# Kernel tuning notes

Measured on AMD Instinct MI355X. Metric: run time of the kernel, lower is better.

Reference implementation:

```python
import jax, jax.numpy as jnp
import numpy as np

B, S_SRC, S_TGT = 32, 128, 128
V, E, H = 32000, 256, 256
PAD_ID = 0
NEG = -1.0e9


def setup_inputs() -> dict:
    key = jax.random.key(0)
    ks = jax.random.split(key, 16)
    lengths_de = jax.random.randint(ks[0], (B,), S_SRC // 2, S_SRC + 1)
    idx_de = jax.random.randint(ks[1], (B, S_SRC), 1, V)
    pos = jnp.arange(S_SRC)[None, :]
    indices_de = jnp.where(pos < lengths_de[:, None], idx_de, PAD_ID)
    indices_en = jax.random.randint(ks[2], (B, S_TGT), 1, V)
    lengths_en = jnp.full((B,), S_TGT, dtype=jnp.int32)

    sc = 0.02
    def nrm(k, shape):
        return jax.random.normal(k, shape, dtype=jnp.float32) * sc
    emb_enc = nrm(ks[3], (V, E)).at[PAD_ID].set(0.0)
    emb_dec = nrm(ks[4], (V, E)).at[PAD_ID].set(0.0)
    return {
        "indices_de": indices_de, "lengths_de": lengths_de,
        "indices_en": indices_en, "lengths_en": lengths_en,
        "emb_enc": emb_enc, "emb_dec": emb_dec,
        "W_ih_enc": nrm(ks[5], (H, E)), "W_hh_enc": nrm(ks[6], (H, H)),
        "b_ih_enc": jnp.zeros((H,), jnp.float32), "b_hh_enc": jnp.zeros((H,), jnp.float32),
        "W_ih_dec": nrm(ks[7], (H, E)), "W_hh_dec": nrm(ks[8], (H, H)),
        "b_ih_dec": jnp.zeros((H,), jnp.float32), "b_hh_dec": jnp.zeros((H,), jnp.float32),
        "W_attn": nrm(ks[9], (H, 2 * H)), "b_attn": jnp.zeros((H,), jnp.float32),
        "W_out": nrm(ks[10], (V, H)), "b_out": jnp.zeros((V,), jnp.float32),
    }


def reference(indices_de, lengths_de, indices_en, lengths_en,
              emb_enc, emb_dec,
              W_ih_enc, W_hh_enc, b_ih_enc, b_hh_enc,
              W_ih_dec, W_hh_dec, b_ih_dec, b_hh_dec,
              W_attn, b_attn, W_out, b_out):
    # ---- Encoder: tanh RNN over packed sequence ----
    x_enc = emb_enc[indices_de]                      # [B, S, E]
    valid = jnp.arange(S_SRC)[None, :] < lengths_de[:, None]  # [B, S]

    def enc_step(h, inp):
        x_t, v_t = inp                                # [B,E], [B]
        h_new = jnp.tanh(x_t @ W_ih_enc.T + b_ih_enc + h @ W_hh_enc.T + b_hh_enc)
        h = jnp.where(v_t[:, None], h_new, h)         # frozen past length (pack semantics)
        out = jnp.where(v_t[:, None], h_new, 0.0)     # padded outputs are zero
        return h, out

    h0 = jnp.zeros((B, H), jnp.float32)
    h_final, enc_outs = jax.lax.scan(
        enc_step, h0, (x_enc.transpose(1, 0, 2), valid.T))
    encoder_outputs = enc_outs.transpose(1, 0, 2)     # [B, S, H]
    enc_mask = indices_de == PAD_ID                   # [B, S] True at padding

    # ---- Decoder: per-step RNN cell + dot-product attention + vocab proj ----
    x_dec = emb_dec[indices_en]                       # [B, T, E]

    def dec_step(h, x_t):
        h = jnp.tanh(x_t @ W_ih_dec.T + b_ih_dec + h @ W_hh_dec.T + b_hh_dec)
        scores = jnp.einsum('bh,bsh->bs', h, encoder_outputs)
        scores = jnp.where(enc_mask, NEG, scores)
        attn = jax.nn.softmax(scores, axis=-1)
        context = jnp.einsum('bs,bsh->bh', attn, encoder_outputs)
        combined = jnp.concatenate([context, h], axis=1)          # [B, 2H]
        attn_out = jnp.tanh(combined @ W_attn.T + b_attn)         # [B, H]
        logits_t = attn_out @ W_out.T + b_out                     # [B, V]
        return h, logits_t

    _, logits = jax.lax.scan(dec_step, h_final, x_dec.transpose(1, 0, 2))
    return logits.transpose(1, 0, 2)                  # [B, T, V]
```

## Files before the change

kernel.cpp:

```cpp
#include <hip/hip_runtime.h>
#include <stdint.h>

#define B_ 32
#define S_ 128
#define T_ 128
#define V_ 32000
#define E_ 256
#define H_ 256
#define NEG_ (-1.0e9f)

typedef __attribute__((ext_vector_type(8))) short short8;
typedef __attribute__((ext_vector_type(4))) float floatx4;

__device__ __forceinline__ unsigned short f2bf(float x){
  unsigned u = __float_as_uint(x);
  u = u + 0x7fffu + ((u >> 16) & 1u);
  return (unsigned short)(u >> 16);
}
__device__ __forceinline__ float bf2f(unsigned short s){
  return __uint_as_float(((unsigned)s) << 16);
}
__device__ __forceinline__ float hsum4(float4 v){ return (v.x+v.y)+(v.z+v.w); }
__device__ __forceinline__ void unpack8(uint4 q, float4& lo, float4& hi){
  lo.x = __uint_as_float(q.x << 16); lo.y = __uint_as_float(q.x & 0xffff0000u);
  lo.z = __uint_as_float(q.y << 16); lo.w = __uint_as_float(q.y & 0xffff0000u);
  hi.x = __uint_as_float(q.z << 16); hi.y = __uint_as_float(q.z & 0xffff0000u);
  hi.z = __uint_as_float(q.w << 16); hi.w = __uint_as_float(q.w & 0xffff0000u);
}

#define GLOAD_LDS16(gptr, lptr) \
  __builtin_amdgcn_global_load_lds( \
      (const __attribute__((address_space(1))) unsigned int*)(const void*)(gptr), \
      (__attribute__((address_space(3))) unsigned int*)(void*)(lptr), 16, 0, 0)

__global__ void k_cvt(const float* __restrict__ src, unsigned short* __restrict__ dst, int n4){
  int i = blockIdx.x*256 + threadIdx.x;
  if (i < n4){
    float4 v = ((const float4*)src)[i];
    ushort4 o; o.x=f2bf(v.x); o.y=f2bf(v.y); o.z=f2bf(v.z); o.w=f2bf(v.w);
    ((ushort4*)dst)[i] = o;
  }
}

__global__ __launch_bounds__(256) void k_xih(
    const int* __restrict__ idxmat,
    const float* __restrict__ emb,
    const float* __restrict__ Wih,
    const float* __restrict__ b1, const float* __restrict__ b2,
    float* __restrict__ out)
{
  __shared__ int idx_s[16];
  __shared__ float4 x_s[16][64];
  int b = blockIdx.x >> 3;
  int t0 = (blockIdx.x & 7) << 4;
  int tid = threadIdx.x;
  if (tid < 16) idx_s[tid] = idxmat[b*128 + t0 + tid];
  __syncthreads();
  for (int r = 0; r < 16; ++r)
    ((float*)&x_s[r][0])[tid] = emb[(size_t)idx_s[r]*E_ + tid];
  __syncthreads();
  int j2 = tid & 127, tg = tid >> 7;
  const float4* W0 = (const float4*)(Wih + (size_t)j2*E_);
  const float4* W1 = (const float4*)(Wih + (size_t)(j2+128)*E_);
  float4 a0[8], a1[8];
  #pragma unroll
  for (int t=0;t<8;++t){ a0[t]={0,0,0,0}; a1[t]={0,0,0,0}; }
  for (int e4 = 0; e4 < 64; ++e4){
    float4 w0 = W0[e4], w1 = W1[e4];
    #pragma unroll
    for (int t = 0; t < 8; ++t){
      float4 xv = x_s[tg*8+t][e4];
      a0[t] += w0*xv; a1[t] += w1*xv;
    }
  }
  float bi0 = b1[j2] + b2[j2];
  float bi1 = b1[j2+128] + b2[j2+128];
  #pragma unroll
  for (int t = 0; t < 8; ++t){
    size_t row = (size_t)((b<<7) + t0 + tg*8 + t)*H_;
    out[row + j2]     = hsum4(a0[t]) + bi0;
    out[row + j2+128] = hsum4(a1[t]) + bi1;
  }
}

template<int ENC>
__global__ __launch_bounds__(512, 2) void k_rnn(
    const float* __restrict__ Whh,
    const float* __restrict__ Xih,
    const float* __restrict__ h0,
    const int* __restrict__ lengths,
    unsigned short* __restrict__ enc_out,
    float* __restrict__ hseq,
    float* __restrict__ hfinal)
{
  __shared__ float4 h4_s[64];
  __shared__ float part[2][256];
  float* h_s = (float*)h4_s;
  int b = blockIdx.x, tid = threadIdx.x;
  int j = tid & 255, half = tid >> 8;
  float4 w[32];
  const float4* Wr = (const float4*)(Whh + (size_t)j*H_ + half*128);
  #pragma unroll
  for (int i = 0; i < 32; ++i) w[i] = Wr[i];
  if (tid < 256) h_s[tid] = ENC ? 0.f : h0[b*H_ + tid];
  int len = ENC ? lengths[b] : T_;
  __syncthreads();
  for (int t = 0; t < 128; ++t){
    float x = 0.f;
    if (tid < 256) x = Xih[(size_t)((b<<7) + t)*H_ + j];
    const float4* hh = h4_s + (half << 5);
    float4 acc0 = {0,0,0,0}, acc1 = {0,0,0,0};
    #pragma unroll
    for (int i = 0; i < 32; i += 2){ acc0 += w[i]*hh[i]; acc1 += w[i+1]*hh[i+1]; }
    part[half][j] = hsum4(acc0) + hsum4(acc1);
    __syncthreads();
    if (tid < 256){
      float s = x + part[0][tid] + part[1][tid];
      float hn = tanhf(s);
      if (ENC){
        float hold = h_s[tid];
        bool v = (t < len);
        h_s[tid] = v ? hn : hold;
        enc_out[(size_t)((b<<7)+t)*H_ + tid] = f2bf(v ? hn : 0.f);
      } else {
        h_s[tid] = hn;
        hseq[(size_t)((b<<7)+t)*H_ + tid] = hn;
      }
    }
    __syncthreads();
  }
  if (ENC && tid < 256) hfinal[b*H_ + tid] = h_s[tid];
}

__global__ __launch_bounds__(256) void k_attn(
    const unsigned short* __restrict__ enc_out,
    const float* __restrict__ hseq,
    const int* __restrict__ lengths,
    const unsigned short* __restrict__ Wattn,
    const float* __restrict__ battn,
    unsigned short* __restrict__ attn_out)
{
  __shared__ float h_sm[16][256];
  __shared__ float sc[16][132];
  __shared__ float comb[16][512];
  int bx = blockIdx.x; int b = bx >> 3; int t0 = (bx & 7) << 4;
  int tid = threadIdx.x;
  int len = lengths[b];
  for (int r = 0; r < 16; ++r)
    h_sm[r][tid] = hseq[(size_t)((b<<7) + t0 + r)*H_ + tid];
  __syncthreads();
  {
    int s = tid & 127, tg = tid >> 7;
    float4 a[8];
    #pragma unroll
    for (int t=0;t<8;++t) a[t] = {0,0,0,0};
    const uint4* ep = (const uint4*)(enc_out + (size_t)(b*S_ + s)*H_);
    for (int oct = 0; oct < 32; ++oct){
      uint4 q = ep[oct];
      float4 elo, ehi; unpack8(q, elo, ehi);
      #pragma unroll
      for (int t = 0; t < 8; ++t){
        const float4* hp = (const float4*)&h_sm[tg*8+t][oct*8];
        a[t] += elo*hp[0] + ehi*hp[1];
      }
    }
    #pragma unroll
    for (int t = 0; t < 8; ++t)
      sc[tg*8+t][s] = (s < len) ? hsum4(a[t]) : NEG_;
  }
  __syncthreads();
  {
    int wv = tid >> 6, ln = tid & 63;
    for (int r = 0; r < 4; ++r){
      int t = r*4 + wv;
      float v0 = sc[t][ln], v1 = sc[t][ln+64];
      float m = fmaxf(v0, v1);
      #pragma unroll
      for (int off = 32; off >= 1; off >>= 1) m = fmaxf(m, __shfl_xor(m, off));
      float e0 = __expf(v0 - m), e1 = __expf(v1 - m);
      float su = e0 + e1;
      #pragma unroll
      for (int off = 32; off >= 1; off >>= 1) su += __shfl_xor(su, off);
      float inv = 1.0f / su;
      sc[t][ln] = e0*inv; sc[t][ln+64] = e1*inv;
    }
  }
  __syncthreads();
  {
    int hd = tid & 127, tg = tid >> 7;
    float c0[8], c1[8];
    #pragma unroll
    for (int t=0;t<8;++t){ c0[t]=0.f; c1[t]=0.f; }
    for (int s4 = 0; s4 < 32; ++s4){
      float ea[4], eb[4];
      #pragma unroll
      for (int i = 0; i < 4; ++i){
        const unsigned short* er = enc_out + (size_t)(b*S_ + s4*4 + i)*H_;
        ea[i] = bf2f(er[hd]); eb[i] = bf2f(er[hd+128]);
      }
      #pragma unroll
      for (int t = 0; t < 8; ++t){
        float4 av = *(const float4*)&sc[tg*8+t][s4*4];
        c0[t] += av.x*ea[0] + av.y*ea[1] + av.z*ea[2] + av.w*ea[3];
        c1[t] += av.x*eb[0] + av.y*eb[1] + av.z*eb[2] + av.w*eb[3];
      }
    }
    #pragma unroll
    for (int t = 0; t < 8; ++t){
      comb[tg*8+t][hd]     = c0[t];
      comb[tg*8+t][hd+128] = c1[t];
    }
  }
  for (int r = 0; r < 16; ++r) comb[r][256 + tid] = h_sm[r][tid];
  __syncthreads();
  {
    int j2 = tid & 127, tg = tid >> 7;
    float4 a0[8], a1[8];
    #pragma unroll
    for (int t=0;t<8;++t){ a0[t]={0,0,0,0}; a1[t]={0,0,0,0}; }
    const uint4* W0 = (const uint4*)(Wattn + (size_t)j2*512);
    const uint4* W1 = (const uint4*)(Wattn + (size_t)(j2+128)*512);
    for (int oct = 0; oct < 64; ++oct){
      float4 w0lo, w0hi, w1lo, w1hi;
      unpack8(W0[oct], w0lo, w0hi);
      unpack8(W1[oct], w1lo, w1hi);
      #pragma unroll
      for (int t = 0; t < 8; ++t){
        const float4* cp = (const float4*)&comb[tg*8+t][oct*8];
        float4 clo = cp[0], chi = cp[1];
        a0[t] += w0lo*clo + w0hi*chi;
        a1[t] += w1lo*clo + w1hi*chi;
      }
    }
    float bi0 = battn[j2], bi1 = battn[j2+128];
    #pragma unroll
    for (int t = 0; t < 8; ++t){
      size_t row = (size_t)((b<<7) + t0 + tg*8 + t)*H_;
      attn_out[row + j2]     = f2bf(tanhf(hsum4(a0[t]) + bi0));
      attn_out[row + j2+128] = f2bf(tanhf(hsum4(a1[t]) + bi1));
    }
  }
}

__global__ __launch_bounds__(256) void k_vocab(
    const unsigned short* __restrict__ A,
    const unsigned short* __restrict__ Wb,
    const float* __restrict__ bout,
    float* __restrict__ out)
{
  __shared__ unsigned short Asm[2][128*32];
  __shared__ unsigned short Bsm[2][128*32];
  int nb = blockIdx.x, mb = blockIdx.y;
  int tid = threadIdx.x;
  int ln  = tid & 63;
  int wid = tid >> 6;
  int llo = ln & 15, lhi = ln >> 4;
  int wr = wid >> 1, wc = wid & 1;
  int mbase = mb*128, nbase = nb*128;

  int c0 = tid, c1 = tid + 256;
  int r0 = c0 >> 2, s0 = (c0 & 3) ^ ((r0 >> 1) & 3);
  int r1 = c1 >> 2, s1 = (c1 & 3) ^ ((r1 >> 1) & 3);
  const unsigned short* Ag0 = A  + (size_t)(mbase + r0)*256 + s0*8;
  const unsigned short* Ag1 = A  + (size_t)(mbase + r1)*256 + s1*8;
  const unsigned short* Bg0 = Wb + (size_t)(nbase + r0)*256 + s0*8;
  const unsigned short* Bg1 = Wb + (size_t)(nbase + r1)*256 + s1*8;

#define STAGE_V(bufi, kk) do { \
    GLOAD_LDS16(Ag0 + (kk), &Asm[bufi][c0*8]); \
    GLOAD_LDS16(Ag1 + (kk), &Asm[bufi][c1*8]); \
    GLOAD_LDS16(Bg0 + (kk), &Bsm[bufi][c0*8]); \
    GLOAD_LDS16(Bg1 + (kk), &Bsm[bufi][c1*8]); \
  } while(0)

  floatx4 acc[4][4];
  #pragma unroll
  for (int mi=0;mi<4;++mi)
    #pragma unroll
    for (int ni=0;ni<4;++ni) acc[mi][ni] = (floatx4){0.f,0.f,0.f,0.f};

  int q = (llo >> 1) & 3;
  int aoff[4], boff[4];
  #pragma unroll
  for (int i=0;i<4;++i){
    int arow = wr*64 + i*16 + llo;
    aoff[i] = arow*32 + ((lhi ^ q)*8);
    int brow = wc*64 + i*16 + llo;
    boff[i] = brow*32 + ((lhi ^ q)*8);
  }

  STAGE_V(0, 0);
  __syncthreads();

  #pragma unroll
  for (int k0 = 0; k0 < 8; ++k0){
    int cur = k0 & 1;
    if (k0 < 7) STAGE_V(cur^1, (k0+1)*32);
    short8 afr[4];
    #pragma unroll
    for (int mi=0;mi<4;++mi)
      afr[mi] = *(const short8*)&Asm[cur][aoff[mi]];
    #pragma unroll
    for (int ni=0;ni<4;++ni){
      short8 bfr = *(const short8*)&Bsm[cur][boff[ni]];
      #pragma unroll
      for (int mi=0;mi<4;++mi)
        acc[mi][ni] = __builtin_amdgcn_mfma_f32_16x16x32_bf16(afr[mi], bfr, acc[mi][ni], 0, 0, 0);
    }
    __syncthreads();
  }

  #pragma unroll
  for (int ni = 0; ni < 4; ++ni){
    int col = nbase + wc*64 + ni*16 + llo;
    float bias = bout[col];
    #pragma unroll
    for (int mi = 0; mi < 4; ++mi){
      #pragma unroll
      for (int r = 0; r < 4; ++r){
        int row = mbase + wr*64 + mi*16 + lhi*4 + r;
        out[(size_t)row*V_ + col] = acc[mi][ni][r] + bias;
      }
    }
  }
#undef STAGE_V
}

extern "C" void kernel_launch(void* const* d_in, const int* in_sizes, int n_in,
                              void* d_out, int out_size, void* d_ws, size_t ws_size,
                              hipStream_t stream){
  const int*   indices_de = (const int*)d_in[0];
  const int*   lengths_de = (const int*)d_in[1];
  const int*   indices_en = (const int*)d_in[2];
  const float* emb_enc   = (const float*)d_in[4];
  const float* emb_dec   = (const float*)d_in[5];
  const float* W_ih_enc  = (const float*)d_in[6];
  const float* W_hh_enc  = (const float*)d_in[7];
  const float* b_ih_enc  = (const float*)d_in[8];
  const float* b_hh_enc  = (const float*)d_in[9];
  const float* W_ih_dec  = (const float*)d_in[10];
  const float* W_hh_dec  = (const float*)d_in[11];
  const float* b_ih_dec  = (const float*)d_in[12];
  const float* b_hh_dec  = (const float*)d_in[13];
  const float* W_attn    = (const float*)d_in[14];
  const float* b_attn    = (const float*)d_in[15];
  const float* W_out     = (const float*)d_in[16];
  const float* b_out     = (const float*)d_in[17];

  char* ws = (char*)d_ws;
  size_t o = 0;
  float* Xih_enc = (float*)(ws + o); o += (size_t)4096*256*4;
  float* Xih_dec = (float*)(ws + o); o += (size_t)4096*256*4;
  unsigned short* enc_bf = (unsigned short*)(ws + o); o += (size_t)4096*256*2;
  float* hfinal  = (float*)(ws + o); o += (size_t)32*256*4;
  float* hdec    = (float*)(ws + o); o += (size_t)4096*256*4;
  unsigned short* attn_o  = (unsigned short*)(ws + o); o += (size_t)4096*256*2;
  unsigned short* Wout_bf = (unsigned short*)(ws + o); o += (size_t)V_*256*2;
  unsigned short* Wattn_bf= (unsigned short*)(ws + o); o += (size_t)256*512*2;

  k_cvt<<<8000, 256, 0, stream>>>(W_out, Wout_bf, 2048000);
  k_cvt<<<128, 256, 0, stream>>>(W_attn, Wattn_bf, 32768);
  k_xih<<<256, 256, 0, stream>>>(indices_de, emb_enc, W_ih_enc, b_ih_enc, b_hh_enc, Xih_enc);
  k_xih<<<256, 256, 0, stream>>>(indices_en, emb_dec, W_ih_dec, b_ih_dec, b_hh_dec, Xih_dec);
  k_rnn<1><<<32, 512, 0, stream>>>(W_hh_enc, Xih_enc, nullptr, lengths_de, enc_bf, nullptr, hfinal);
  k_rnn<0><<<32, 512, 0, stream>>>(W_hh_dec, Xih_dec, hfinal, nullptr, nullptr, hdec, nullptr);
  k_attn<<<256, 256, 0, stream>>>(enc_bf, hdec, lengths_de, Wattn_bf, b_attn, attn_o);
  dim3 gD(250, 32);
  k_vocab<<<gD, 256, 0, stream>>>(attn_o, Wout_bf, b_out, (float*)d_out);
}
```

Baseline: 995.0 us.

## Merge prep and RNN launches, enlarge vocab GEMM tile with XCD-aware mapping

Folds the two weight conversions and the two input-projection kernels into one launch, with the block index choosing the work. Runs the encoder and decoder recurrences in a single kernel, so the hidden state passes through shared memory instead of a global hfinal buffer. The per-step barriers become a manual waitcnt plus s_barrier. The vocab GEMM moves to 512-thread blocks with 256x128 tiles on a 1D grid, grouping M-blocks by XCD so each XCD can reuse W_out in L2. The larger tile and block size may reduce occupancy.

```diff
diff --git a/kernel.cpp b/kernel.cpp
--- a/kernel.cpp
+++ b/kernel.cpp
@@ -33,8 +33,15 @@
       (const __attribute__((address_space(1))) unsigned int*)(const void*)(gptr), \
       (__attribute__((address_space(3))) unsigned int*)(void*)(lptr), 16, 0, 0)
 
-__global__ void k_cvt(const float* __restrict__ src, unsigned short* __restrict__ dst, int n4){
-  int i = blockIdx.x*256 + threadIdx.x;
+#define LDS_BARRIER() do { \
+    asm volatile("s_waitcnt lgkmcnt(0)" ::: "memory"); \
+    __builtin_amdgcn_s_barrier(); \
+  } while(0)
+
+__device__ __forceinline__ void cvt_body(const float* __restrict__ src,
+                                         unsigned short* __restrict__ dst,
+                                         int blk, int n4){
+  int i = blk*256 + (int)threadIdx.x;
   if (i < n4){
     float4 v = ((const float4*)src)[i];
     ushort4 o; o.x=f2bf(v.x); o.y=f2bf(v.y); o.z=f2bf(v.z); o.w=f2bf(v.w);
@@ -42,17 +49,15 @@
   }
 }
 
-__global__ __launch_bounds__(256) void k_xih(
-    const int* __restrict__ idxmat,
-    const float* __restrict__ emb,
+__device__ __forceinline__ void xih_body(
+    const int* __restrict__ idxmat, const float* __restrict__ emb,
     const float* __restrict__ Wih,
     const float* __restrict__ b1, const float* __restrict__ b2,
-    float* __restrict__ out)
+    float* __restrict__ out, int blk,
+    int* idx_s, float4 (*x_s)[64])
 {
-  __shared__ int idx_s[16];
-  __shared__ float4 x_s[16][64];
-  int b = blockIdx.x >> 3;
-  int t0 = (blockIdx.x & 7) << 4;
+  int b = blk >> 3;
+  int t0 = (blk & 7) << 4;
   int tid = threadIdx.x;
   if (tid < 16) idx_s[tid] = idxmat[b*128 + t0 + tid];
   __syncthreads();
@@ -83,15 +88,38 @@
   }
 }
 
-template<int ENC>
-__global__ __launch_bounds__(512, 2) void k_rnn(
-    const float* __restrict__ Whh,
-    const float* __restrict__ Xih,
-    const float* __restrict__ h0,
+__global__ __launch_bounds__(256) void k_prep(
+    const float* __restrict__ W_out, unsigned short* __restrict__ Wout_bf,
+    const float* __restrict__ W_attn, unsigned short* __restrict__ Wattn_bf,
+    const int* __restrict__ indices_de, const float* __restrict__ emb_enc,
+    const float* __restrict__ W_ih_enc, const float* __restrict__ b_ih_enc,
+    const float* __restrict__ b_hh_enc, float* __restrict__ Xih_enc,
+    const int* __restrict__ indices_en, const float* __restrict__ emb_dec,
+    const float* __restrict__ W_ih_dec, const float* __restrict__ b_ih_dec,
+    const float* __restrict__ b_hh_dec, float* __restrict__ Xih_dec)
+{
+  __shared__ int idx_s[16];
+  __shared__ float4 x_s[16][64];
+  int bx = blockIdx.x;
+  if (bx < 8000){
+    cvt_body(W_out, Wout_bf, bx, 2048000);
+  } else if (bx < 8128){
+    cvt_body(W_attn, Wattn_bf, bx - 8000, 32768);
+  } else if (bx < 8384){
+    xih_body(indices_de, emb_enc, W_ih_enc, b_ih_enc, b_hh_enc, Xih_enc,
+             bx - 8128, idx_s, x_s);
+  } else {
+    xih_body(indices_en, emb_dec, W_ih_dec, b_ih_dec, b_hh_dec, Xih_dec,
+             bx - 8384, idx_s, x_s);
+  }
+}
+
+__global__ __launch_bounds__(512, 2) void k_rnn2(
+    const float* __restrict__ Whh_e, const float* __restrict__ Whh_d,
+    const float* __restrict__ Xih_e, const float* __restrict__ Xih_d,
     const int* __restrict__ lengths,
     unsigned short* __restrict__ enc_out,
-    float* __restrict__ hseq,
-    float* __restrict__ hfinal)
+    float* __restrict__ hseq)
 {
   __shared__ float4 h4_s[64];
   __shared__ float part[2][256];
@@ -99,37 +127,53 @@
   int b = blockIdx.x, tid = threadIdx.x;
   int j = tid & 255, half = tid >> 8;
   float4 w[32];
-  const float4* Wr = (const float4*)(Whh + (size_t)j*H_ + half*128);
+  const float4* Wr = (const float4*)(Whh_e + (size_t)j*H_ + half*128);
   #pragma unroll
   for (int i = 0; i < 32; ++i) w[i] = Wr[i];
-  if (tid < 256) h_s[tid] = ENC ? 0.f : h0[b*H_ + tid];
-  int len = ENC ? lengths[b] : T_;
-  __syncthreads();
+  if (tid < 256) h_s[tid] = 0.f;
+  int len = lengths[b];
+  __syncthreads();
+
   for (int t = 0; t < 128; ++t){
     float x = 0.f;
-    if (tid < 256) x = Xih[(size_t)((b<<7) + t)*H_ + j];
+    if (tid < 256) x = Xih_e[(size_t)((b<<7) + t)*H_ + j];
     const float4* hh = h4_s + (half << 5);
     float4 acc0 = {0,0,0,0}, acc1 = {0,0,0,0};
     #pragma unroll
     for (int i = 0; i < 32; i += 2){ acc0 += w[i]*hh[i]; acc1 += w[i+1]*hh[i+1]; }
     part[half][j] = hsum4(acc0) + hsum4(acc1);
-    __syncthreads();
+    LDS_BARRIER();
     if (tid < 256){
       float s = x + part[0][tid] + part[1][tid];
       float hn = tanhf(s);
-      if (ENC){
-        float hold = h_s[tid];
-        bool v = (t < len);
-        h_s[tid] = v ? hn : hold;
-        enc_out[(size_t)((b<<7)+t)*H_ + tid] = f2bf(v ? hn : 0.f);
-      } else {
-        h_s[tid] = hn;
-        hseq[(size_t)((b<<7)+t)*H_ + tid] = hn;
-      }
-    }
-    __syncthreads();
-  }
-  if (ENC && tid < 256) hfinal[b*H_ + tid] = h_s[tid];
+      float hold = h_s[tid];
+      bool v = (t < len);
+      h_s[tid] = v ? hn : hold;
+      enc_out[(size_t)((b<<7)+t)*H_ + tid] = f2bf(v ? hn : 0.f);
+    }
+    LDS_BARRIER();
+  }
+
+  Wr = (const float4*)(Whh_d + (size_t)j*H_ + half*128);
+  #pragma unroll
+  for (int i = 0; i < 32; ++i) w[i] = Wr[i];
+  for (int t = 0; t < 128; ++t){
+    float x = 0.f;
+    if (tid < 256) x = Xih_d[(size_t)((b<<7) + t)*H_ + j];
+    const float4* hh = h4_s + (half << 5);
+    float4 acc0 = {0,0,0,0}, acc1 = {0,0,0,0};
+    #pragma unroll
+    for (int i = 0; i < 32; i += 2){ acc0 += w[i]*hh[i]; acc1 += w[i+1]*hh[i+1]; }
+    part[half][j] = hsum4(acc0) + hsum4(acc1);
+    LDS_BARRIER();
+    if (tid < 256){
+      float s = x + part[0][tid] + part[1][tid];
+      float hn = tanhf(s);
+      h_s[tid] = hn;
+      hseq[(size_t)((b<<7)+t)*H_ + tid] = hn;
+    }
+    LDS_BARRIER();
+  }
 }
 
 __global__ __launch_bounds__(256) void k_attn(
@@ -242,35 +286,37 @@
   }
 }
 
-__global__ __launch_bounds__(256) void k_vocab(
+__global__ __launch_bounds__(512) void k_vocab(
     const unsigned short* __restrict__ A,
     const unsigned short* __restrict__ Wb,
     const float* __restrict__ bout,
     float* __restrict__ out)
 {
-  __shared__ unsigned short Asm[2][128*32];
-  __shared__ unsigned short Bsm[2][128*32];
-  int nb = blockIdx.x, mb = blockIdx.y;
+  __shared__ alignas(16) unsigned short Asm[2][256*32];
+  __shared__ alignas(16) unsigned short Bsm[2][128*32];
+  int bid = blockIdx.x;
+  int xcd = bid & 7, idx = bid >> 3;
+  int nb = idx >> 1;
+  int mb = (xcd << 1) | (idx & 1);
   int tid = threadIdx.x;
   int ln  = tid & 63;
   int wid = tid >> 6;
   int llo = ln & 15, lhi = ln >> 4;
   int wr = wid >> 1, wc = wid & 1;
-  int mbase = mb*128, nbase = nb*128;
-
-  int c0 = tid, c1 = tid + 256;
-  int r0 = c0 >> 2, s0 = (c0 & 3) ^ ((r0 >> 1) & 3);
-  int r1 = c1 >> 2, s1 = (c1 & 3) ^ ((r1 >> 1) & 3);
-  const unsigned short* Ag0 = A  + (size_t)(mbase + r0)*256 + s0*8;
-  const unsigned short* Ag1 = A  + (size_t)(mbase + r1)*256 + s1*8;
-  const unsigned short* Bg0 = Wb + (size_t)(nbase + r0)*256 + s0*8;
-  const unsigned short* Bg1 = Wb + (size_t)(nbase + r1)*256 + s1*8;
+  int mbase = mb*256, nbase = nb*128;
+
+  int ca0 = tid, ca1 = tid + 512, cb = tid;
+  int ra0 = ca0 >> 2, sa0 = (ca0 & 3) ^ ((ra0 >> 1) & 3);
+  int ra1 = ca1 >> 2, sa1 = (ca1 & 3) ^ ((ra1 >> 1) & 3);
+  int rb  = cb  >> 2, sb  = (cb  & 3) ^ ((rb  >> 1) & 3);
+  const unsigned short* Ag0 = A  + (size_t)(mbase + ra0)*256 + sa0*8;
+  const unsigned short* Ag1 = A  + (size_t)(mbase + ra1)*256 + sa1*8;
+  const unsigned short* Bg  = Wb + (size_t)(nbase + rb )*256 + sb*8;
 
 #define STAGE_V(bufi, kk) do { \
-    GLOAD_LDS16(Ag0 + (kk), &Asm[bufi][c0*8]); \
-    GLOAD_LDS16(Ag1 + (kk), &Asm[bufi][c1*8]); \
-    GLOAD_LDS16(Bg0 + (kk), &Bsm[bufi][c0*8]); \
-    GLOAD_LDS16(Bg1 + (kk), &Bsm[bufi][c1*8]); \
+    GLOAD_LDS16(Ag0 + (kk), &Asm[bufi][ca0*8]); \
+    GLOAD_LDS16(Ag1 + (kk), &Asm[bufi][ca1*8]); \
+    GLOAD_LDS16(Bg  + (kk), &Bsm[bufi][cb*8]); \
   } while(0)
 
   floatx4 acc[4][4];
@@ -283,14 +329,13 @@
   int aoff[4], boff[4];
   #pragma unroll
   for (int i=0;i<4;++i){
-    int arow = wr*64 + i*16 + llo;
-    aoff[i] = arow*32 + ((lhi ^ q)*8);
-    int brow = wc*64 + i*16 + llo;
-    boff[i] = brow*32 + ((lhi ^ q)*8);
+    aoff[i] = (wr*64 + i*16 + llo)*32 + ((lhi ^ q)*8);
+    boff[i] = (wc*64 + i*16 + llo)*32 + ((lhi ^ q)*8);
   }
 
   STAGE_V(0, 0);
-  __syncthreads();
+  asm volatile("s_waitcnt vmcnt(0)" ::: "memory");
+  __builtin_amdgcn_s_barrier();
 
   #pragma unroll
   for (int k0 = 0; k0 < 8; ++k0){
@@ -307,7 +352,8 @@
       for (int mi=0;mi<4;++mi)
         acc[mi][ni] = __builtin_amdgcn_mfma_f32_16x16x32_bf16(afr[mi], bfr, acc[mi][ni], 0, 0, 0);
     }
-    __syncthreads();
+    asm volatile("s_waitcnt vmcnt(0)" ::: "memory");
+    __builtin_amdgcn_s_barrier();
   }
 
   #pragma unroll
@@ -352,19 +398,17 @@
   float* Xih_enc = (float*)(ws + o); o += (size_t)4096*256*4;
   float* Xih_dec = (float*)(ws + o); o += (size_t)4096*256*4;
   unsigned short* enc_bf = (unsigned short*)(ws + o); o += (size_t)4096*256*2;
-  float* hfinal  = (float*)(ws + o); o += (size_t)32*256*4;
   float* hdec    = (float*)(ws + o); o += (size_t)4096*256*4;
   unsigned short* attn_o  = (unsigned short*)(ws + o); o += (size_t)4096*256*2;
   unsigned short* Wout_bf = (unsigned short*)(ws + o); o += (size_t)V_*256*2;
   unsigned short* Wattn_bf= (unsigned short*)(ws + o); o += (size_t)256*512*2;
 
-  k_cvt<<<8000, 256, 0, stream>>>(W_out, Wout_bf, 2048000);
-  k_cvt<<<128, 256, 0, stream>>>(W_attn, Wattn_bf, 32768);
-  k_xih<<<256, 256, 0, stream>>>(indices_de, emb_enc, W_ih_enc, b_ih_enc, b_hh_enc, Xih_enc);
-  k_xih<<<256, 256, 0, stream>>>(indices_en, emb_dec, W_ih_dec, b_ih_dec, b_hh_dec, Xih_dec);
-  k_rnn<1><<<32, 512, 0, stream>>>(W_hh_enc, Xih_enc, nullptr, lengths_de, enc_bf, nullptr, hfinal);
-  k_rnn<0><<<32, 512, 0, stream>>>(W_hh_dec, Xih_dec, hfinal, nullptr, nullptr, hdec, nullptr);
+  k_prep<<<8640, 256, 0, stream>>>(
+      W_out, Wout_bf, W_attn, Wattn_bf,
+      indices_de, emb_enc, W_ih_enc, b_ih_enc, b_hh_enc, Xih_enc,
+      indices_en, emb_dec, W_ih_dec, b_ih_dec, b_hh_dec, Xih_dec);
+  k_rnn2<<<32, 512, 0, stream>>>(W_hh_enc, W_hh_dec, Xih_enc, Xih_dec,
+                                 lengths_de, enc_bf, hdec);
   k_attn<<<256, 256, 0, stream>>>(enc_bf, hdec, lengths_de, Wattn_bf, b_attn, attn_o);
-  dim3 gD(250, 32);
-  k_vocab<<<gD, 256, 0, stream>>>(attn_o, Wout_bf, b_out, (float*)d_out);
-}
+  k_vocab<<<4000, 512, 0, stream>>>(attn_o, Wout_bf, b_out, (float*)d_out);
+}
```

Result: no change. 1.002 ms (+0.7%).
